# Kernel optimization log

Measured on AMD Instinct MI355X. Metric: run time of the kernel, lower is better.

Reference implementation:

```python
import jax, jax.numpy as jnp
import numpy as np

N_NODES = 50000


def gcn_layer(x, src, dst, ew, W, b, n_nodes):
    # PyG GCNConv: add self-loops (weight 1), symmetric deg^-1/2 normalization,
    # linear transform, scatter-add aggregation at destination, then bias.
    loop = jnp.arange(n_nodes, dtype=src.dtype)
    s = jnp.concatenate([src, loop])
    d = jnp.concatenate([dst, loop])
    w = jnp.concatenate([ew, jnp.ones((n_nodes,), dtype=ew.dtype)])
    deg = jax.ops.segment_sum(w, d, num_segments=n_nodes)  # [N]
    dinv = jnp.where(deg > 0, jax.lax.rsqrt(jnp.where(deg > 0, deg, 1.0)), 0.0)
    norm = dinv[s] * w * dinv[d]  # [E+N]
    h = x @ W  # [N, out]
    msg = h[s] * norm[:, None]  # gather + scale, [E+N, out]
    out = jax.ops.segment_sum(msg, d, num_segments=n_nodes)  # scatter-add
    return out + b


def setup_inputs() -> dict:
    key = jax.random.key(0)
    k1, k2, k3, k4, k5, k6, k7 = jax.random.split(key, 7)
    N, E, C_IN, C_OUT = N_NODES, 600000, 128, 128
    x = jax.random.normal(k1, (N, C_IN), dtype=jnp.float32)
    edge_index = jax.random.randint(k2, (2, E), 0, N, dtype=jnp.int64)
    edge_weight = jax.random.uniform(k3, (E,), dtype=jnp.float32)
    # Glorot-style init like PyG's Linear default
    s1 = 1.0 / np.sqrt(C_IN)
    s2 = 1.0 / np.sqrt(C_OUT)
    W1 = jax.random.uniform(k4, (C_IN, C_OUT), jnp.float32, -s1, s1)
    b1 = jnp.zeros((C_OUT,), dtype=jnp.float32)
    W2 = jax.random.uniform(k5, (C_OUT, C_OUT), jnp.float32, -s2, s2)
    b2 = jnp.zeros((C_OUT,), dtype=jnp.float32)
    return {"x": x, "edge_index": edge_index, "edge_weight": edge_weight,
            "W1": W1, "b1": b1, "W2": W2, "b2": b2}


def reference(x, edge_index, edge_weight, W1, b1, W2, b2):
    src, dst = edge_index[0], edge_index[1]
    h = jax.nn.relu(gcn_layer(x, src, dst, edge_weight, W1, b1, N_NODES))
    return jax.nn.relu(gcn_layer(h, src, dst, edge_weight, W2, b2, N_NODES))
```

## Files before the change

### kernel.cpp

```cpp
#include <hip/hip_runtime.h>
#include <math.h>

#define CH   128
#define CH4  32
#define TPB  256
#define SCANB 1024
#define WIMG 16384

typedef __attribute__((ext_vector_type(8))) short short8;
typedef __attribute__((ext_vector_type(4))) float floatx4;

static __device__ __forceinline__ unsigned short f2bf(float f) {
    unsigned u = __float_as_uint(f);
    return (unsigned short)((u + 0x7fffu + ((u >> 16) & 1u)) >> 16);
}
static __device__ __forceinline__ float bf2f(unsigned short s) {
    return __uint_as_float(((unsigned)s) << 16);
}
static __device__ __forceinline__ float4 bf4_to_f4(ushort4 u) {
    return make_float4(bf2f(u.x), bf2f(u.y), bf2f(u.z), bf2f(u.w));
}

__global__ void k_prep(const float* __restrict__ W1, const float* __restrict__ W2,
                       short* __restrict__ Wsplit) {
    int i = blockIdx.x * blockDim.x + threadIdx.x;
    if (i >= 2 * CH * CH) return;
    int layer = i >> 14;
    int idx   = i & 16383;
    int k = idx >> 7, c = idx & 127;
    float w = (layer ? W2 : W1)[k * CH + c];
    unsigned short hi = f2bf(w);
    unsigned short lo = f2bf(w - bf2f(hi));
    int colh = c >> 6, nn = c & 63;
    int kt = k >> 5, q = (k & 31) >> 3, j = k & 7;
    int ns = nn >> 4, ln = q * 16 + (nn & 15);
    size_t base = (size_t)(layer * 2 + colh) * WIMG;
    size_t off  = ((size_t)(kt * 4 + ns) * 64 + ln) * 8 + j;
    Wsplit[base + off]        = (short)hi;
    Wsplit[base + 8192 + off] = (short)lo;
}

template<int RELU_IN>
static __device__ __forceinline__ void gemm_body(
        const float* __restrict__ X, const short* __restrict__ Wfrag,
        unsigned short* __restrict__ H, int n, int tile, int colh, int tid) {
    __shared__ __align__(16) short sW[2][4][4][64][8];
    {
        const float4* gsrc = (const float4*)Wfrag;
        float4* ldst = (float4*)sW;
        #pragma unroll
        for (int i = 0; i < 8; ++i)
            ldst[i * TPB + tid] = gsrc[i * TPB + tid];
    }
    __syncthreads();

    const int lane = tid & 63;
    const int wv   = tid >> 6;
    const int q    = lane >> 4;
    const int m    = lane & 15;
    const int row0 = tile * 64 + wv * 16;
    if (row0 >= n) return;

    int rrow = row0 + m;
    if (rrow > n - 1) rrow = n - 1;

    const float4* xr = (const float4*)(X + (size_t)rrow * CH);
    float4 xa[4][2];
    #pragma unroll
    for (int kt = 0; kt < 4; ++kt) {
        xa[kt][0] = xr[kt * 8 + q * 2 + 0];
        xa[kt][1] = xr[kt * 8 + q * 2 + 1];
    }

    floatx4 acc[4];
    #pragma unroll
    for (int ns = 0; ns < 4; ++ns) acc[ns] = (floatx4){0.f, 0.f, 0.f, 0.f};

    #pragma unroll
    for (int kt = 0; kt < 4; ++kt) {
        float xf[8] = { xa[kt][0].x, xa[kt][0].y, xa[kt][0].z, xa[kt][0].w,
                        xa[kt][1].x, xa[kt][1].y, xa[kt][1].z, xa[kt][1].w };
        short8 ah, al;
        #pragma unroll
        for (int j = 0; j < 8; ++j) {
            float v = xf[j];
            if (RELU_IN) v = fmaxf(v, 0.f);
            unsigned short h = f2bf(v);
            ah[j] = (short)h;
            al[j] = (short)f2bf(v - bf2f(h));
        }
        #pragma unroll
        for (int ns = 0; ns < 4; ++ns) {
            short8 bh = *(const short8*)&sW[0][kt][ns][lane][0];
            short8 bl = *(const short8*)&sW[1][kt][ns][lane][0];
            acc[ns] = __builtin_amdgcn_mfma_f32_16x16x32_bf16(ah, bh, acc[ns], 0, 0, 0);
            acc[ns] = __builtin_amdgcn_mfma_f32_16x16x32_bf16(al, bh, acc[ns], 0, 0, 0);
            acc[ns] = __builtin_amdgcn_mfma_f32_16x16x32_bf16(ah, bl, acc[ns], 0, 0, 0);
        }
    }

    #pragma unroll
    for (int ns = 0; ns < 4; ++ns) {
        #pragma unroll
        for (int reg = 0; reg < 4; ++reg) {
            int r = row0 + q * 4 + reg;
            if (r < n)
                H[(size_t)r * CH + colh * 64 + ns * 16 + m] = f2bf(acc[ns][reg]);
        }
    }
}

template<int RELU_IN>
__global__ __launch_bounds__(TPB, 4)
void k_gemm(const float* __restrict__ X, const short* __restrict__ Wsplit,
            unsigned short* __restrict__ H, int n) {
    int colh = (int)blockIdx.x & 1;
    gemm_body<RELU_IN>(X, Wsplit + (size_t)colh * WIMG, H, n,
                       (int)blockIdx.x >> 1, colh, threadIdx.x);
}

__global__ __launch_bounds__(TPB, 4)
void k_gemm_rank(const float* __restrict__ X, const short* __restrict__ Wsplit,
                 unsigned short* __restrict__ H, int n,
                 const int* __restrict__ dst, int* __restrict__ counts,
                 int* __restrict__ rank, int E, int nbE) {
    int bx = blockIdx.x;
    if (bx < nbE) {
        int e = bx * TPB + threadIdx.x;
        if (e < E) {
            int d = dst[e];
            if ((unsigned)d < (unsigned)n)
                rank[e] = atomicAdd(&counts[d], 1);
        }
    } else {
        bx -= nbE;
        int colh = bx & 1;
        gemm_body<0>(X, Wsplit + (size_t)colh * WIMG, H, n, bx >> 1, colh,
                     threadIdx.x);
    }
}

__global__ __launch_bounds__(SCANB)
void k_scan1(const int* __restrict__ counts, int* __restrict__ row_start,
             int* __restrict__ partials, int n) {
    __shared__ int s[SCANB];
    int gid = blockIdx.x * SCANB + threadIdx.x;
    int v = (gid < n) ? counts[gid] : 0;
    s[threadIdx.x] = v;
    __syncthreads();
    for (int off = 1; off < SCANB; off <<= 1) {
        int t = (threadIdx.x >= off) ? s[threadIdx.x - off] : 0;
        __syncthreads();
        s[threadIdx.x] += t;
        __syncthreads();
    }
    if (gid < n) row_start[gid] = s[threadIdx.x] - v;
    if (threadIdx.x == SCANB - 1) partials[blockIdx.x] = s[SCANB - 1];
}

__global__ __launch_bounds__(64)
void k_scan2(int* __restrict__ partials, int nb) {
    __shared__ int s[64];
    int v = (threadIdx.x < nb) ? partials[threadIdx.x] : 0;
    s[threadIdx.x] = v;
    __syncthreads();
    for (int off = 1; off < 64; off <<= 1) {
        int t = (threadIdx.x >= off) ? s[threadIdx.x - off] : 0;
        __syncthreads();
        s[threadIdx.x] += t;
        __syncthreads();
    }
    if (threadIdx.x < nb) partials[threadIdx.x] = s[threadIdx.x] - v;
}

__global__ __launch_bounds__(SCANB)
void k_scan3(int* __restrict__ row_start, const int* __restrict__ partials, int n) {
    int gid = blockIdx.x * SCANB + threadIdx.x;
    if (gid < n) row_start[gid] += partials[blockIdx.x];
}

__global__ void k_fill(const int* __restrict__ src, const int* __restrict__ dst,
                       const float* __restrict__ ew, const int* __restrict__ row_start,
                       const int* __restrict__ rank, int2* __restrict__ edges,
                       int E, int n) {
    int e = blockIdx.x * blockDim.x + threadIdx.x;
    if (e >= E) return;
    int s = src[e], d = dst[e];
    if ((unsigned)s >= (unsigned)n || (unsigned)d >= (unsigned)n) return;
    edges[row_start[d] + rank[e]] = make_int2(s, __float_as_int(ew[e]));
}

__global__ void k_deg(const int* __restrict__ row_start, const int* __restrict__ counts,
                      const int2* __restrict__ edges, float* __restrict__ dinv, int n) {
    int i = blockIdx.x * blockDim.x + threadIdx.x;
    if (i >= n) return;
    int j = row_start[i], end = j + counts[i];
    float sum = 1.0f;
    for (; j < end; ++j) sum += __int_as_float(edges[j].y);
    dinv[i] = rsqrtf(sum);
}

template<int RELU_OUT, int FIXUP>
__global__ __launch_bounds__(TPB)
void k_aggregate(const unsigned short* __restrict__ h, const int* __restrict__ row_start,
                 const int* __restrict__ counts, int2* __restrict__ edges,
                 const float* __restrict__ dinv, const float* __restrict__ bias,
                 float* __restrict__ out, int n) {
    int t = blockIdx.x * blockDim.x + threadIdx.x;
    int node = t >> 5;
    if (node >= n) return;
    int tx = t & 31;

    const ushort4* h4 = (const ushort4*)h;
    float di = dinv[node];
    float4 b  = ((const float4*)bias)[tx];
    float4 hv = bf4_to_f4(h4[(size_t)node * CH4 + tx]);
    float4 acc = make_float4(0.f, 0.f, 0.f, 0.f);

    int j   = row_start[node];
    int end = j + counts[node];

    for (; j + 8 <= end; j += 8) {
        int2 e[8];
        #pragma unroll
        for (int i = 0; i < 8; ++i) e[i] = edges[j + i];
        ushort4 g[8];
        #pragma unroll
        for (int i = 0; i < 8; ++i) g[i] = h4[(size_t)e[i].x * CH4 + tx];
        float w[8];
        #pragma unroll
        for (int i = 0; i < 8; ++i) {
            w[i] = __int_as_float(e[i].y);
            if (FIXUP) w[i] *= dinv[e[i].x];
        }
        if (FIXUP && tx == 0) {
            #pragma unroll
            for (int i = 0; i < 8; ++i) edges[j + i].y = __float_as_int(w[i]);
        }
        #pragma unroll
        for (int i = 0; i < 8; ++i) {
            float4 gf = bf4_to_f4(g[i]);
            acc.x += gf.x * w[i]; acc.y += gf.y * w[i];
            acc.z += gf.z * w[i]; acc.w += gf.w * w[i];
        }
    }
    if (j + 4 <= end) {
        int2 e[4];
        #pragma unroll
        for (int i = 0; i < 4; ++i) e[i] = edges[j + i];
        ushort4 g[4];
        #pragma unroll
        for (int i = 0; i < 4; ++i) g[i] = h4[(size_t)e[i].x * CH4 + tx];
        float w[4];
        #pragma unroll
        for (int i = 0; i < 4; ++i) {
            w[i] = __int_as_float(e[i].y);
            if (FIXUP) w[i] *= dinv[e[i].x];
        }
        if (FIXUP && tx == 0) {
            #pragma unroll
            for (int i = 0; i < 4; ++i) edges[j + i].y = __float_as_int(w[i]);
        }
        #pragma unroll
        for (int i = 0; i < 4; ++i) {
            float4 gf = bf4_to_f4(g[i]);
            acc.x += gf.x * w[i]; acc.y += gf.y * w[i];
            acc.z += gf.z * w[i]; acc.w += gf.w * w[i];
        }
        j += 4;
    }
    for (; j < end; ++j) {
        int2 e0 = edges[j];
        float w0 = __int_as_float(e0.y);
        if (FIXUP) w0 *= dinv[e0.x];
        if (FIXUP && tx == 0) edges[j].y = __float_as_int(w0);
        float4 gf = bf4_to_f4(h4[(size_t)e0.x * CH4 + tx]);
        acc.x += gf.x * w0; acc.y += gf.y * w0;
        acc.z += gf.z * w0; acc.w += gf.w * w0;
    }

    float sc = di * di;
    float4 o = make_float4(hv.x * sc + b.x + di * acc.x,
                           hv.y * sc + b.y + di * acc.y,
                           hv.z * sc + b.z + di * acc.z,
                           hv.w * sc + b.w + di * acc.w);
    if (RELU_OUT) {
        o.x = fmaxf(o.x, 0.f); o.y = fmaxf(o.y, 0.f);
        o.z = fmaxf(o.z, 0.f); o.w = fmaxf(o.w, 0.f);
    }
    ((float4*)out)[(size_t)node * CH4 + tx] = o;
}

extern "C" void kernel_launch(void* const* d_in, const int* in_sizes, int n_in,
                              void* d_out, int out_size, void* d_ws, size_t ws_size,
                              hipStream_t stream) {
    const float* x  = (const float*)d_in[0];
    const int*   ei = (const int*)d_in[1];
    const float* ew = (const float*)d_in[2];
    const float* W1 = (const float*)d_in[3];
    const float* b1 = (const float*)d_in[4];
    const float* W2 = (const float*)d_in[5];
    const float* b2 = (const float*)d_in[6];
    float* out = (float*)d_out;

    const int N = in_sizes[0] / CH;
    const int E = in_sizes[2];
    const int* src = ei;
    const int* dst = ei + E;

    size_t Np = ((size_t)N + 255) & ~(size_t)255;
    float* ws        = (float*)d_ws;
    float* dinv      = ws;
    unsigned short* h = (unsigned short*)(dinv + Np);
    int*   counts    = (int*)(h + (size_t)N * CH);
    int*   row_start = counts + Np;
    int*   rank      = row_start + Np;
    int*   partials  = rank + (((size_t)E + 63) & ~(size_t)63);
    int2*  edges     = (int2*)(partials + 64);
    short* Wsplit    = (short*)(edges + E);

    const int nbN    = (N + TPB - 1) / TPB;
    const int nbE    = (E + TPB - 1) / TPB;
    const int nbAgg  = (int)(((size_t)N * 32 + TPB - 1) / TPB);
    const int nbScan = (N + SCANB - 1) / SCANB;
    const int nbGemm2 = 2 * ((N + 63) / 64);
    const int nbPrep  = (2 * CH * CH + TPB - 1) / TPB;

    hipMemsetAsync(counts, 0, (size_t)N * sizeof(int), stream);
    k_prep     <<<nbPrep, TPB, 0, stream>>>(W1, W2, Wsplit);

    k_gemm_rank<<<nbE + nbGemm2, TPB, 0, stream>>>(x, Wsplit, h, N, dst,
                                                   counts, rank, E, nbE);
    k_scan1    <<<nbScan, SCANB, 0, stream>>>(counts, row_start, partials, N);
    k_scan2    <<<1, 64, 0, stream>>>(partials, nbScan);
    k_scan3    <<<nbScan, SCANB, 0, stream>>>(row_start, partials, N);
    k_fill     <<<nbE, TPB, 0, stream>>>(src, dst, ew, row_start, rank, edges, E, N);
    k_deg      <<<nbN, TPB, 0, stream>>>(row_start, counts, edges, dinv, N);

    k_aggregate<0,1><<<nbAgg, TPB, 0, stream>>>(h, row_start, counts, edges,
                                                dinv, b1, out, N);
    k_gemm<1>       <<<nbGemm2, TPB, 0, stream>>>(out, Wsplit + 2 * WIMG, h, N);
    k_aggregate<1,0><<<nbAgg, TPB, 0, stream>>>(h, row_start, counts, edges,
                                                dinv, b2, out, N);
}
```

Measured before the change: 230.6 us.

## Store layer-1 output as bf16, replicate degree counters, merge scan passes

Layer 1 aggregation now applies ReLU and writes its output in bf16. The second GEMM reads that bf16 input directly and issues two MFMAs per tile instead of three, dropping the low-part split of the activations. The edge rank counting spreads its atomics over four replicated counter arrays to reduce contention, with per-replica offsets computed in the scan. The separate scan2 kernel is removed and each scan3 block reduces the partials itself. This saves memory traffic, MFMA work and one launch, at the cost of extra precision loss in layer 2's input and more counter memory to clear.

```diff
diff --git a/kernel.cpp b/kernel.cpp
--- a/kernel.cpp
+++ b/kernel.cpp
@@ -6,6 +6,7 @@
 #define TPB  256
 #define SCANB 1024
 #define WIMG 16384
+#define NREP 4
 
 typedef __attribute__((ext_vector_type(8))) short short8;
 typedef __attribute__((ext_vector_type(4))) float floatx4;
@@ -40,18 +41,20 @@
     Wsplit[base + 8192 + off] = (short)lo;
 }
 
-template<int RELU_IN>
-static __device__ __forceinline__ void gemm_body(
+#define STAGE_W(sW, Wfrag, tid)                                    \
+    {                                                              \
+        const float4* gsrc = (const float4*)(Wfrag);               \
+        float4* ldst = (float4*)(sW);                              \
+        _Pragma("unroll")                                          \
+        for (int i = 0; i < 8; ++i)                                \
+            ldst[i * TPB + (tid)] = gsrc[i * TPB + (tid)];         \
+    }
+
+static __device__ __forceinline__ void gemm_body_f32(
         const float* __restrict__ X, const short* __restrict__ Wfrag,
         unsigned short* __restrict__ H, int n, int tile, int colh, int tid) {
     __shared__ __align__(16) short sW[2][4][4][64][8];
-    {
-        const float4* gsrc = (const float4*)Wfrag;
-        float4* ldst = (float4*)sW;
-        #pragma unroll
-        for (int i = 0; i < 8; ++i)
-            ldst[i * TPB + tid] = gsrc[i * TPB + tid];
-    }
+    STAGE_W(sW, Wfrag, tid);
     __syncthreads();
 
     const int lane = tid & 63;
@@ -84,7 +87,6 @@
         #pragma unroll
         for (int j = 0; j < 8; ++j) {
             float v = xf[j];
-            if (RELU_IN) v = fmaxf(v, 0.f);
             unsigned short h = f2bf(v);
             ah[j] = (short)h;
             al[j] = (short)f2bf(v - bf2f(h));
@@ -110,42 +112,106 @@
     }
 }
 
-template<int RELU_IN>
-__global__ __launch_bounds__(TPB, 4)
-void k_gemm(const float* __restrict__ X, const short* __restrict__ Wsplit,
-            unsigned short* __restrict__ H, int n) {
-    int colh = (int)blockIdx.x & 1;
-    gemm_body<RELU_IN>(X, Wsplit + (size_t)colh * WIMG, H, n,
-                       (int)blockIdx.x >> 1, colh, threadIdx.x);
+static __device__ __forceinline__ void gemm_body_bf(
+        const unsigned short* __restrict__ X, const short* __restrict__ Wfrag,
+        unsigned short* __restrict__ H, int n, int tile, int colh, int tid) {
+    __shared__ __align__(16) short sW[2][4][4][64][8];
+    STAGE_W(sW, Wfrag, tid);
+    __syncthreads();
+
+    const int lane = tid & 63;
+    const int wv   = tid >> 6;
+    const int q    = lane >> 4;
+    const int m    = lane & 15;
+    const int row0 = tile * 64 + wv * 16;
+    if (row0 >= n) return;
+
+    int rrow = row0 + m;
+    if (rrow > n - 1) rrow = n - 1;
+
+    const ushort4* xr = (const ushort4*)(X + (size_t)rrow * CH);
+    short8 a[4];
+    #pragma unroll
+    for (int kt = 0; kt < 4; ++kt) {
+        ushort4 u0 = xr[kt * 8 + q * 2 + 0];
+        ushort4 u1 = xr[kt * 8 + q * 2 + 1];
+        a[kt][0] = (short)u0.x; a[kt][1] = (short)u0.y;
+        a[kt][2] = (short)u0.z; a[kt][3] = (short)u0.w;
+        a[kt][4] = (short)u1.x; a[kt][5] = (short)u1.y;
+        a[kt][6] = (short)u1.z; a[kt][7] = (short)u1.w;
+    }
+
+    floatx4 acc[4];
+    #pragma unroll
+    for (int ns = 0; ns < 4; ++ns) acc[ns] = (floatx4){0.f, 0.f, 0.f, 0.f};
+
+    #pragma unroll
+    for (int kt = 0; kt < 4; ++kt) {
+        #pragma unroll
+        for (int ns = 0; ns < 4; ++ns) {
+            short8 bh = *(const short8*)&sW[0][kt][ns][lane][0];
+            short8 bl = *(const short8*)&sW[1][kt][ns][lane][0];
+            acc[ns] = __builtin_amdgcn_mfma_f32_16x16x32_bf16(a[kt], bh, acc[ns], 0, 0, 0);
+            acc[ns] = __builtin_amdgcn_mfma_f32_16x16x32_bf16(a[kt], bl, acc[ns], 0, 0, 0);
+        }
+    }
+
+    #pragma unroll
+    for (int ns = 0; ns < 4; ++ns) {
+        #pragma unroll
+        for (int reg = 0; reg < 4; ++reg) {
+            int r = row0 + q * 4 + reg;
+            if (r < n)
+                H[(size_t)r * CH + colh * 64 + ns * 16 + m] = f2bf(acc[ns][reg]);
+        }
+    }
 }
 
 __global__ __launch_bounds__(TPB, 4)
 void k_gemm_rank(const float* __restrict__ X, const short* __restrict__ Wsplit,
                  unsigned short* __restrict__ H, int n,
-                 const int* __restrict__ dst, int* __restrict__ counts,
-                 int* __restrict__ rank, int E, int nbE) {
+                 const int* __restrict__ dst, int* __restrict__ counts_rep,
+                 int* __restrict__ rank, int E, int nbE, int Np) {
     int bx = blockIdx.x;
     if (bx < nbE) {
         int e = bx * TPB + threadIdx.x;
         if (e < E) {
             int d = dst[e];
-            if ((unsigned)d < (unsigned)n)
-                rank[e] = atomicAdd(&counts[d], 1);
+            if ((unsigned)d < (unsigned)n) {
+                int rep = e & (NREP - 1);
+                rank[e] = atomicAdd(&counts_rep[rep * Np + d], 1);
+            }
         }
     } else {
         bx -= nbE;
         int colh = bx & 1;
-        gemm_body<0>(X, Wsplit + (size_t)colh * WIMG, H, n, bx >> 1, colh,
-                     threadIdx.x);
-    }
+        gemm_body_f32(X, Wsplit + (size_t)colh * WIMG, H, n, bx >> 1, colh,
+                      threadIdx.x);
+    }
+}
+
+__global__ __launch_bounds__(TPB, 4)
+void k_gemm_bf(const unsigned short* __restrict__ X, const short* __restrict__ Wsplit,
+               unsigned short* __restrict__ H, int n) {
+    int colh = (int)blockIdx.x & 1;
+    gemm_body_bf(X, Wsplit + (size_t)colh * WIMG, H, n,
+                 (int)blockIdx.x >> 1, colh, threadIdx.x);
 }
 
 __global__ __launch_bounds__(SCANB)
-void k_scan1(const int* __restrict__ counts, int* __restrict__ row_start,
-             int* __restrict__ partials, int n) {
+void k_scan1(const int* __restrict__ counts_rep, int Np,
+             int* __restrict__ counts_tot, int4* __restrict__ repoff,
+             int* __restrict__ row_start, int* __restrict__ partials, int n) {
     __shared__ int s[SCANB];
     int gid = blockIdx.x * SCANB + threadIdx.x;
-    int v = (gid < n) ? counts[gid] : 0;
+    int c0 = 0, c1 = 0, c2 = 0, c3 = 0;
+    if (gid < n) {
+        c0 = counts_rep[gid];
+        c1 = counts_rep[Np + gid];
+        c2 = counts_rep[2 * Np + gid];
+        c3 = counts_rep[3 * Np + gid];
+    }
+    int v = c0 + c1 + c2 + c3;
     s[threadIdx.x] = v;
     __syncthreads();
     for (int off = 1; off < SCANB; off <<= 1) {
@@ -154,40 +220,40 @@
         s[threadIdx.x] += t;
         __syncthreads();
     }
-    if (gid < n) row_start[gid] = s[threadIdx.x] - v;
+    if (gid < n) {
+        row_start[gid]  = s[threadIdx.x] - v;
+        counts_tot[gid] = v;
+        repoff[gid]     = make_int4(0, c0, c0 + c1, c0 + c1 + c2);
+    }
     if (threadIdx.x == SCANB - 1) partials[blockIdx.x] = s[SCANB - 1];
-}
-
-__global__ __launch_bounds__(64)
-void k_scan2(int* __restrict__ partials, int nb) {
-    __shared__ int s[64];
-    int v = (threadIdx.x < nb) ? partials[threadIdx.x] : 0;
-    s[threadIdx.x] = v;
-    __syncthreads();
-    for (int off = 1; off < 64; off <<= 1) {
-        int t = (threadIdx.x >= off) ? s[threadIdx.x - off] : 0;
-        __syncthreads();
-        s[threadIdx.x] += t;
-        __syncthreads();
-    }
-    if (threadIdx.x < nb) partials[threadIdx.x] = s[threadIdx.x] - v;
 }
 
 __global__ __launch_bounds__(SCANB)
 void k_scan3(int* __restrict__ row_start, const int* __restrict__ partials, int n) {
+    __shared__ int sbase;
+    if (threadIdx.x < 64) {
+        int v = (threadIdx.x < blockIdx.x) ? partials[threadIdx.x] : 0;
+        #pragma unroll
+        for (int off = 32; off; off >>= 1) v += __shfl_down(v, off, 64);
+        if (threadIdx.x == 0) sbase = v;
+    }
+    __syncthreads();
     int gid = blockIdx.x * SCANB + threadIdx.x;
-    if (gid < n) row_start[gid] += partials[blockIdx.x];
+    if (gid < n) row_start[gid] += sbase;
 }
 
 __global__ void k_fill(const int* __restrict__ src, const int* __restrict__ dst,
                        const float* __restrict__ ew, const int* __restrict__ row_start,
-                       const int* __restrict__ rank, int2* __restrict__ edges,
-                       int E, int n) {
+                       const int4* __restrict__ repoff, const int* __restrict__ rank,
+                       int2* __restrict__ edges, int E, int n) {
     int e = blockIdx.x * blockDim.x + threadIdx.x;
     if (e >= E) return;
     int s = src[e], d = dst[e];
     if ((unsigned)s >= (unsigned)n || (unsigned)d >= (unsigned)n) return;
-    edges[row_start[d] + rank[e]] = make_int2(s, __float_as_int(ew[e]));
+    int rep = e & (NREP - 1);
+    int4 ro = repoff[d];
+    int roa[4] = {ro.x, ro.y, ro.z, ro.w};
+    edges[row_start[d] + roa[rep] + rank[e]] = make_int2(s, __float_as_int(ew[e]));
 }
 
 __global__ void k_deg(const int* __restrict__ row_start, const int* __restrict__ counts,
@@ -200,12 +266,12 @@
     dinv[i] = rsqrtf(sum);
 }
 
-template<int RELU_OUT, int FIXUP>
+template<int RELU_OUT, int FIXUP, int OUT_BF16>
 __global__ __launch_bounds__(TPB)
 void k_aggregate(const unsigned short* __restrict__ h, const int* __restrict__ row_start,
                  const int* __restrict__ counts, int2* __restrict__ edges,
                  const float* __restrict__ dinv, const float* __restrict__ bias,
-                 float* __restrict__ out, int n) {
+                 void* __restrict__ out, int n) {
     int t = blockIdx.x * blockDim.x + threadIdx.x;
     int node = t >> 5;
     if (node >= n) return;
@@ -288,7 +354,12 @@
         o.x = fmaxf(o.x, 0.f); o.y = fmaxf(o.y, 0.f);
         o.z = fmaxf(o.z, 0.f); o.w = fmaxf(o.w, 0.f);
     }
-    ((float4*)out)[(size_t)node * CH4 + tx] = o;
+    if (OUT_BF16) {
+        ushort4 u = make_ushort4(f2bf(o.x), f2bf(o.y), f2bf(o.z), f2bf(o.w));
+        ((ushort4*)out)[(size_t)node * CH4 + tx] = u;
+    } else {
+        ((float4*)out)[(size_t)node * CH4 + tx] = o;
+    }
 }
 
 extern "C" void kernel_launch(void* const* d_in, const int* in_sizes, int n_in,
@@ -309,15 +380,19 @@
     const int* dst = ei + E;
 
     size_t Np = ((size_t)N + 255) & ~(size_t)255;
-    float* ws        = (float*)d_ws;
-    float* dinv      = ws;
-    unsigned short* h = (unsigned short*)(dinv + Np);
-    int*   counts    = (int*)(h + (size_t)N * CH);
-    int*   row_start = counts + Np;
-    int*   rank      = row_start + Np;
-    int*   partials  = rank + (((size_t)E + 63) & ~(size_t)63);
-    int2*  edges     = (int2*)(partials + 64);
-    short* Wsplit    = (short*)(edges + E);
+    size_t Ep = ((size_t)E + 63) & ~(size_t)63;
+    float* ws          = (float*)d_ws;
+    float* dinv        = ws;
+    unsigned short* h  = (unsigned short*)(dinv + Np);
+    unsigned short* o1 = h + (size_t)N * CH;
+    int*  counts_rep   = (int*)(o1 + (size_t)N * CH);
+    int*  counts_tot   = counts_rep + NREP * Np;
+    int*  row_start    = counts_tot + Np;
+    int4* repoff       = (int4*)(row_start + Np);
+    int*  rank         = (int*)(repoff + Np);
+    int*  partials     = rank + Ep;
+    int2* edges        = (int2*)(partials + 64);
+    short* Wsplit      = (short*)(edges + E);
 
     const int nbN    = (N + TPB - 1) / TPB;
     const int nbE    = (E + TPB - 1) / TPB;
@@ -326,20 +401,21 @@
     const int nbGemm2 = 2 * ((N + 63) / 64);
     const int nbPrep  = (2 * CH * CH + TPB - 1) / TPB;
 
-    hipMemsetAsync(counts, 0, (size_t)N * sizeof(int), stream);
+    hipMemsetAsync(counts_rep, 0, (size_t)NREP * Np * sizeof(int), stream);
     k_prep     <<<nbPrep, TPB, 0, stream>>>(W1, W2, Wsplit);
 
     k_gemm_rank<<<nbE + nbGemm2, TPB, 0, stream>>>(x, Wsplit, h, N, dst,
-                                                   counts, rank, E, nbE);
-    k_scan1    <<<nbScan, SCANB, 0, stream>>>(counts, row_start, partials, N);
-    k_scan2    <<<1, 64, 0, stream>>>(partials, nbScan);
+                                                   counts_rep, rank, E, nbE, (int)Np);
+    k_scan1    <<<nbScan, SCANB, 0, stream>>>(counts_rep, (int)Np, counts_tot,
+                                              repoff, row_start, partials, N);
     k_scan3    <<<nbScan, SCANB, 0, stream>>>(row_start, partials, N);
-    k_fill     <<<nbE, TPB, 0, stream>>>(src, dst, ew, row_start, rank, edges, E, N);
-    k_deg      <<<nbN, TPB, 0, stream>>>(row_start, counts, edges, dinv, N);
-
-    k_aggregate<0,1><<<nbAgg, TPB, 0, stream>>>(h, row_start, counts, edges,
-                                                dinv, b1, out, N);
-    k_gemm<1>       <<<nbGemm2, TPB, 0, stream>>>(out, Wsplit + 2 * WIMG, h, N);
-    k_aggregate<1,0><<<nbAgg, TPB, 0, stream>>>(h, row_start, counts, edges,
-                                                dinv, b2, out, N);
-}
+    k_fill     <<<nbE, TPB, 0, stream>>>(src, dst, ew, row_start, repoff, rank,
+                                         edges, E, N);
+    k_deg      <<<nbN, TPB, 0, stream>>>(row_start, counts_tot, edges, dinv, N);
+
+    k_aggregate<1,1,1><<<nbAgg, TPB, 0, stream>>>(h, row_start, counts_tot, edges,
+                                                  dinv, b1, o1, N);
+    k_gemm_bf         <<<nbGemm2, TPB, 0, stream>>>(o1, Wsplit + 2 * WIMG, h, N);
+    k_aggregate<1,0,0><<<nbAgg, TPB, 0, stream>>>(h, row_start, counts_tot, edges,
+                                                  dinv, b2, out, N);
+}
```

Result: faster. 224.4 us (-2.7%).
